# Optimization experiments

Measured on AMD Instinct MI355X. Metric: run time of the kernel, lower is better.

The kernel has to match this reference:

```python
import jax, jax.numpy as jnp
import numpy as np
import math

RC = 3.6            # cutoff radius
SMOOTH_W = 0.3      # ShiftedCosine smoothing width
N_RAD = 12          # max_radial=11 -> 12 radial functions
L_MAX = 3           # max_angular
N_TYPES = 3
BOX = 27.4
# neighbor-type pairs a1<=a2 (keys_to_properties layout), sqrt(2) for off-diagonal
PAIR_A1 = np.array([0, 0, 0, 1, 1, 2])
PAIR_A2 = np.array([0, 1, 2, 1, 2, 2])
PAIR_FACT = np.where(PAIR_A1 != PAIR_A2, np.sqrt(2.0), 1.0).astype(np.float32)


def _gto_setup():
    # GTO primitives g_n(r) = N_n r^n exp(-r^2/(2 sigma_n^2)), orthonormalized via S^{-1/2}
    n = np.arange(N_RAD, dtype=np.float64)
    sigma = RC * np.maximum(np.sqrt(n), 1.0) / N_RAD
    gam = np.array([math.gamma(v) for v in (n + 1.5)])
    norm = 1.0 / np.sqrt(0.5 * gam * sigma ** (2 * n + 3))
    npow = n[:, None] + n[None, :]
    c = 0.5 / sigma[:, None] ** 2 + 0.5 / sigma[None, :] ** 2
    gam2 = np.vectorize(math.gamma)((npow + 3.0) / 2.0)
    S = norm[:, None] * norm[None, :] * 0.5 * gam2 * c ** (-(npow + 3.0) / 2.0)
    w, V = np.linalg.eigh(S)
    Sinv_half = (V * (1.0 / np.sqrt(w))) @ V.T
    return sigma.astype(np.float32), norm.astype(np.float32), Sinv_half.astype(np.float32)

SIGMA, NORM, SINV = _gto_setup()


def radial_basis(r):
    # r [...,] -> [..., N_RAD] orthonormalized GTO values
    n = jnp.arange(N_RAD, dtype=r.dtype)
    sig = jnp.asarray(SIGMA)
    g = jnp.asarray(NORM) * r[..., None] ** n * jnp.exp(-0.5 * r[..., None] ** 2 / sig ** 2)
    return g @ jnp.asarray(SINV)


def real_sph_l3(u):
    # real spherical harmonics l=0..3 on unit vectors u [...,3] -> [...,16]
    x, y, z = u[..., 0], u[..., 1], u[..., 2]
    x2, y2, z2 = x * x, y * y, z * z
    one = jnp.ones_like(x)
    return jnp.stack([
        0.28209479177387814 * one,
        0.4886025119029199 * y, 0.4886025119029199 * z, 0.4886025119029199 * x,
        1.0925484305920792 * x * y, 1.0925484305920792 * y * z,
        0.31539156525252005 * (3.0 * z2 - 1.0),
        1.0925484305920792 * x * z, 0.5462742152960396 * (x2 - y2),
        0.5900435899266435 * y * (3.0 * x2 - y2), 2.890611442640554 * x * y * z,
        0.4570457994644658 * y * (5.0 * z2 - 1.0), 0.3731763325901154 * z * (5.0 * z2 - 3.0),
        0.4570457994644658 * x * (5.0 * z2 - 1.0), 1.445305721320277 * z * (x2 - y2),
        0.5900435899266435 * x * (3.0 * x2 - y2),
    ], axis=-1)


def cutoff_fn(r):
    # ShiftedCosine: 1 for r<rc-w, cosine switch on [rc-w, rc], 0 beyond
    t = jnp.clip((r - (RC - SMOOTH_W)) / SMOOTH_W, 0.0, 1.0)
    return 0.5 * (1.0 + jnp.cos(jnp.pi * t))


def soap_features(positions, species):
    B, N, _ = positions.shape
    rvec = positions[:, :, None, :] - positions[:, None, :, :]  # [B,N,N,3]
    d2 = jnp.sum(rvec * rvec, axis=-1)
    nonself = ~jnp.eye(N, dtype=bool)[None]
    dist = jnp.sqrt(jnp.where(nonself, d2, 1.0))                 # safe for grads
    w = cutoff_fn(dist) * nonself                                 # [B,N,N] pair weight
    unit = rvec / dist[..., None]
    R = radial_basis(dist) * w[..., None]                         # [B,N,N,12]
    Y = real_sph_l3(unit)                                         # [B,N,N,16]
    T = jax.nn.one_hot(species, N_TYPES, dtype=positions.dtype)   # [B,N,3]
    # density expansion coefficients c_{i,a,n,lm}
    c = jnp.einsum('bja,bijn,bijk->biank', T, R, Y)               # [B,N,3,12,16]
    c1 = c[:, :, PAIR_A1]                                         # [B,N,6,12,16]
    c2 = c[:, :, PAIR_A2]
    l_slices = [(0, 1), (1, 4), (4, 9), (9, 16)]
    ps = []
    for l, (s, e) in enumerate(l_slices):
        p = jnp.einsum('bipnm,bipqm->bipnq', c1[..., s:e], c2[..., s:e])
        ps.append(p / jnp.sqrt(jnp.asarray(2.0 * l + 1.0, positions.dtype)))
    p = jnp.stack(ps, axis=-1)                                    # [B,N,6,12,12,4]
    p = p * jnp.asarray(PAIR_FACT)[:, None, None, None]
    return p.reshape(B * N, -1)                                   # [B*N, 3456]


def setup_inputs() -> dict:
    key = jax.random.key(0)
    k0, k1, k2 = jax.random.split(key, 3)
    positions = jax.random.uniform(k0, (4, 1024, 3), dtype=jnp.float32) * BOX
    species = jax.random.randint(k1, (4, 1024), 0, N_TYPES, dtype=jnp.int32)
    W = jax.random.normal(k2, (3456,), dtype=jnp.float32) * 0.02
    b = jnp.zeros((1,), dtype=jnp.float32)
    return {"positions": positions, "species": species, "W": W, "b": b}


def reference(positions, species, W, b):
    feats = soap_features(positions, species)   # [B*N, 3456]
    return feats @ W[:, None] + b               # per-atom energies [B*N, 1]
```

## Files before the change

kernel.cpp:

```cpp
#include <hip/hip_runtime.h>
#include <math.h>

#define NRAD   12
#define NSPH   16
#define NTYPE  3
#define NATOM  1024
#define MAXNBR 64
#define RCUT   3.6f

#define RSTR   13
#define YSTR   17
#define CSTR   20

#define NPAIR  144

#define SQRT2F 1.41421356237309515f
#define LS1    0.57735026918962576f
#define LS2    0.44721359549995794f
#define LS3    0.37796447300922722f

struct SoapConsts {
    float norm[NRAD];
    float inv2sig2[NRAD];
    float sinv[NRAD * NRAD];
};

static void compute_consts(SoapConsts* C) {
    double G[26];
    G[2] = 1.0;
    G[3] = 0.88622692545275801364908374167057259139877;
    for (int t = 4; t < 26; ++t) G[t] = (0.5 * t - 1.0) * G[t - 2];

    double sigma[NRAD], norm[NRAD];
    for (int n = 0; n < NRAD; ++n) {
        double sq = sqrt((double)n);
        if (sq < 1.0) sq = 1.0;
        sigma[n] = 3.6 * sq / 12.0;
        norm[n]  = 1.0 / sqrt(0.5 * G[2 * n + 3] * pow(sigma[n], 2.0 * n + 3.0));
    }

    double S[NRAD][NRAD];
    for (int i = 0; i < NRAD; ++i)
        for (int j = 0; j < NRAD; ++j) {
            double c = 0.5 / (sigma[i] * sigma[i]) + 0.5 / (sigma[j] * sigma[j]);
            double e = 0.5 * (i + j + 3.0);
            S[i][j]  = norm[i] * norm[j] * 0.5 * G[i + j + 3] * pow(c, -e);
        }

    double A[NRAD][NRAD], V[NRAD][NRAD];
    for (int i = 0; i < NRAD; ++i)
        for (int j = 0; j < NRAD; ++j) {
            A[i][j] = S[i][j];
            V[i][j] = (i == j) ? 1.0 : 0.0;
        }
    for (int sweep = 0; sweep < 60; ++sweep) {
        double off = 0.0;
        for (int p = 0; p < NRAD - 1; ++p)
            for (int q = p + 1; q < NRAD; ++q) off += A[p][q] * A[p][q];
        if (off < 1e-26) break;
        for (int p = 0; p < NRAD - 1; ++p) {
            for (int q = p + 1; q < NRAD; ++q) {
                double apq = A[p][q];
                if (fabs(apq) < 1e-300) continue;
                double tau = (A[q][q] - A[p][p]) / (2.0 * apq);
                double tt  = ((tau >= 0.0) ? 1.0 : -1.0) / (fabs(tau) + sqrt(1.0 + tau * tau));
                double cc  = 1.0 / sqrt(1.0 + tt * tt);
                double ss  = tt * cc;
                for (int k = 0; k < NRAD; ++k) {
                    double akp = A[k][p], akq = A[k][q];
                    A[k][p] = cc * akp - ss * akq;
                    A[k][q] = ss * akp + cc * akq;
                }
                for (int k = 0; k < NRAD; ++k) {
                    double apk = A[p][k], aqk = A[q][k];
                    A[p][k] = cc * apk - ss * aqk;
                    A[q][k] = ss * apk + cc * aqk;
                }
                for (int k = 0; k < NRAD; ++k) {
                    double vkp = V[k][p], vkq = V[k][q];
                    V[k][p] = cc * vkp - ss * vkq;
                    V[k][q] = ss * vkp + cc * vkq;
                }
            }
        }
    }
    double wisr[NRAD];
    for (int k = 0; k < NRAD; ++k) wisr[k] = 1.0 / sqrt(A[k][k]);
    for (int i = 0; i < NRAD; ++i)
        for (int j = 0; j < NRAD; ++j) {
            double s = 0.0;
            for (int k = 0; k < NRAD; ++k) s += V[i][k] * wisr[k] * V[j][k];
            C->sinv[i * NRAD + j] = (float)s;
        }
    for (int n = 0; n < NRAD; ++n) {
        C->norm[n]     = (float)norm[n];
        C->inv2sig2[n] = (float)(0.5 / (sigma[n] * sigma[n]));
    }
}

__device__ __forceinline__ void ldrow(const float* __restrict__ row, float* r) {
    const float4* p = reinterpret_cast<const float4*>(row);
    float4 a = p[0], b = p[1], c = p[2], d = p[3];
    r[0]=a.x;  r[1]=a.y;  r[2]=a.z;  r[3]=a.w;
    r[4]=b.x;  r[5]=b.y;  r[6]=b.z;  r[7]=b.w;
    r[8]=c.x;  r[9]=c.y;  r[10]=c.z; r[11]=c.w;
    r[12]=d.x; r[13]=d.y; r[14]=d.z; r[15]=d.w;
}

__device__ __forceinline__ float dot4l(const float* c1, const float* c2,
                                       float4 w4, float fact) {
    float d0 = c1[0]*c2[0];
    float d1 = c1[1]*c2[1] + c1[2]*c2[2] + c1[3]*c2[3];
    float d2 = c1[4]*c2[4] + c1[5]*c2[5] + c1[6]*c2[6] + c1[7]*c2[7]
             + c1[8]*c2[8];
    float d3 = c1[9]*c2[9] + c1[10]*c2[10] + c1[11]*c2[11] + c1[12]*c2[12]
             + c1[13]*c2[13] + c1[14]*c2[14] + c1[15]*c2[15];
    return fact * (w4.x * d0 + (LS1 * w4.y) * d1
                 + (LS2 * w4.z) * d2 + (LS3 * w4.w) * d3);
}

__global__ __launch_bounds__(64) void soap_kernel(
    const float* __restrict__ positions,
    const int*   __restrict__ species,
    const float* __restrict__ W,
    const float* __restrict__ bias,
    float*       __restrict__ out,
    SoapConsts C)
{
    const int atom = blockIdx.x;
    const int b    = atom >> 10;
    const int i    = atom & (NATOM - 1);
    const int lane = threadIdx.x;

    const float* pos = positions + b * NATOM * 3;
    const float xi = pos[3 * i], yi = pos[3 * i + 1], zi = pos[3 * i + 2];

    __shared__ int   nbIdx[MAXNBR];
    __shared__ float nbR[MAXNBR][RSTR];
    __shared__ float nbY[MAXNBR][YSTR];
    __shared__ int   nbSp[MAXNBR];
    __shared__ float cbuf[NTYPE][NRAD * CSTR];

    int nNbr = 0;
    const float rc2 = RCUT * RCUT;
    for (int base = 0; base < NATOM; base += 64) {
        int j = base + lane;
        float dx = xi - pos[3 * j];
        float dy = yi - pos[3 * j + 1];
        float dz = zi - pos[3 * j + 2];
        float d2 = dx * dx + dy * dy + dz * dz;
        bool pred = (j != i) && (d2 < rc2);
        unsigned long long m = __ballot(pred);
        if (pred) {
            int slot = nNbr + __popcll(m & ((1ull << lane) - 1ull));
            if (slot < MAXNBR) nbIdx[slot] = j;
        }
        nNbr += __popcll(m);
    }
    if (nNbr > MAXNBR) nNbr = MAXNBR;
    __syncthreads();

    if (lane < nNbr) {
        int j = nbIdx[lane];
        float dx = xi - pos[3 * j];
        float dy = yi - pos[3 * j + 1];
        float dz = zi - pos[3 * j + 2];
        float d2 = dx * dx + dy * dy + dz * dz;
        float d  = sqrtf(d2);
        float inv = 1.0f / d;
        float ux = dx * inv, uy = dy * inv, uz = dz * inv;

        float t = (d - (RCUT - 0.3f)) * (1.0f / 0.3f);
        t = fminf(fmaxf(t, 0.0f), 1.0f);
        float w = 0.5f * (1.0f + cosf(3.14159265358979323846f * t));

        float g[NRAD];
        float rp = 1.0f;
        #pragma unroll
        for (int n = 0; n < NRAD; ++n) {
            g[n] = C.norm[n] * rp * expf(-d2 * C.inv2sig2[n]) * w;
            rp *= d;
        }
        #pragma unroll
        for (int mm = 0; mm < NRAD; ++mm) {
            float s = 0.0f;
            #pragma unroll
            for (int n = 0; n < NRAD; ++n) s += g[n] * C.sinv[n * NRAD + mm];
            nbR[lane][mm] = s;
        }

        float x2 = ux * ux, y2 = uy * uy, z2 = uz * uz;
        nbY[lane][0]  = 0.28209479177387814f;
        nbY[lane][1]  = 0.4886025119029199f * uy;
        nbY[lane][2]  = 0.4886025119029199f * uz;
        nbY[lane][3]  = 0.4886025119029199f * ux;
        nbY[lane][4]  = 1.0925484305920792f * ux * uy;
        nbY[lane][5]  = 1.0925484305920792f * uy * uz;
        nbY[lane][6]  = 0.31539156525252005f * (3.0f * z2 - 1.0f);
        nbY[lane][7]  = 1.0925484305920792f * ux * uz;
        nbY[lane][8]  = 0.5462742152960396f * (x2 - y2);
        nbY[lane][9]  = 0.5900435899266435f * uy * (3.0f * x2 - y2);
        nbY[lane][10] = 2.890611442640554f * ux * uy * uz;
        nbY[lane][11] = 0.4570457994644658f * uy * (5.0f * z2 - 1.0f);
        nbY[lane][12] = 0.3731763325901154f * uz * (5.0f * z2 - 3.0f);
        nbY[lane][13] = 0.4570457994644658f * ux * (5.0f * z2 - 1.0f);
        nbY[lane][14] = 1.445305721320277f * uz * (x2 - y2);
        nbY[lane][15] = 0.5900435899266435f * ux * (3.0f * x2 - y2);
        nbSp[lane] = species[b * NATOM + j];
    }
    __syncthreads();

    float a0[3], a1_[3], a2_[3];
    int mI[3], kI[3];
    #pragma unroll
    for (int t = 0; t < 3; ++t) {
        a0[t] = a1_[t] = a2_[t] = 0.0f;
        int mk = lane + t * 64;
        mI[t] = mk >> 4;
        kI[t] = mk & 15;
    }
    for (int j = 0; j < nNbr; ++j) {
        int sp = nbSp[j];
        #pragma unroll
        for (int t = 0; t < 3; ++t) {
            float v = nbR[j][mI[t]] * nbY[j][kI[t]];
            a0[t]  += (sp == 0) ? v : 0.0f;
            a1_[t] += (sp == 1) ? v : 0.0f;
            a2_[t] += (sp == 2) ? v : 0.0f;
        }
    }
    #pragma unroll
    for (int t = 0; t < 3; ++t) {
        cbuf[0][mI[t] * CSTR + kI[t]] = a0[t];
        cbuf[1][mI[t] * CSTR + kI[t]] = a1_[t];
        cbuf[2][mI[t] * CSTR + kI[t]] = a2_[t];
    }
    __syncthreads();

    float partial = 0.0f;
    for (int t = 0; t < 3; ++t) {
        int pi  = lane + (t << 6);
        bool act = (pi < NPAIR);
        int piC = act ? pi : 0;
        int n = piC / 12;
        int q = piC - 12 * n;

        float cq0[16], cq1[16], cq2[16], cn_[16];
        ldrow(&cbuf[0][q * CSTR], cq0);
        ldrow(&cbuf[1][q * CSTR], cq1);
        ldrow(&cbuf[2][q * CSTR], cq2);

        const float* wbase = W + n * 48 + q * 4;
        float acc = 0.0f;

        ldrow(&cbuf[0][n * CSTR], cn_);
        acc += dot4l(cn_, cq0, *reinterpret_cast<const float4*>(wbase + 0 * 576), 1.0f);
        acc += dot4l(cn_, cq1, *reinterpret_cast<const float4*>(wbase + 1 * 576), SQRT2F);
        acc += dot4l(cn_, cq2, *reinterpret_cast<const float4*>(wbase + 2 * 576), SQRT2F);

        ldrow(&cbuf[1][n * CSTR], cn_);
        acc += dot4l(cn_, cq1, *reinterpret_cast<const float4*>(wbase + 3 * 576), 1.0f);
        acc += dot4l(cn_, cq2, *reinterpret_cast<const float4*>(wbase + 4 * 576), SQRT2F);

        ldrow(&cbuf[2][n * CSTR], cn_);
        acc += dot4l(cn_, cq2, *reinterpret_cast<const float4*>(wbase + 5 * 576), 1.0f);

        partial += act ? acc : 0.0f;
    }

    #pragma unroll
    for (int off = 32; off > 0; off >>= 1)
        partial += __shfl_down(partial, off, 64);
    if (lane == 0) out[atom] = partial + bias[0];
}

extern "C" void kernel_launch(void* const* d_in, const int* in_sizes, int n_in,
                              void* d_out, int out_size, void* d_ws, size_t ws_size,
                              hipStream_t stream) {
    const float* positions = (const float*)d_in[0];
    const int*   species   = (const int*)d_in[1];
    const float* W         = (const float*)d_in[2];
    const float* bias      = (const float*)d_in[3];
    float*       out       = (float*)d_out;

    SoapConsts C;
    compute_consts(&C);

    int nAtoms = in_sizes[0] / 3;
    soap_kernel<<<nAtoms, 64, 0, stream>>>(positions, species, W, bias, out, C);
}
```

Baseline: 75.73 us.

## Transpose positions to SoA, shrink neighbor cap, and cut register pressure

A new pre-kernel transposes positions into a global SoA buffer so the neighbor scan does coalesced loads. MAXNBR drops from 64 to 32, and the shared arrays lose their padding. Neighbor index and species are packed into one shared int. The pair loop is restructured with unroll 1 and fewer live row arrays, together with launch bounds of 6 waves, to lower register use and raise occupancy. Capping neighbors at 32 can silently drop neighbors in dense regions (the expected count here is about 32 at this density), which changes results, and the extra launch adds overhead.

```diff
diff --git a/kernel.cpp b/kernel.cpp
--- a/kernel.cpp
+++ b/kernel.cpp
@@ -5,11 +5,11 @@
 #define NSPH   16
 #define NTYPE  3
 #define NATOM  1024
-#define MAXNBR 64
+#define MAXNBR 32
 #define RCUT   3.6f
 
-#define RSTR   13
-#define YSTR   17
+#define RSTR   12
+#define YSTR   16
 #define CSTR   20
 
 #define NPAIR  144
@@ -24,6 +24,8 @@
     float inv2sig2[NRAD];
     float sinv[NRAD * NRAD];
 };
+
+__device__ float g_posT[3][4 * NATOM];
 
 static void compute_consts(SoapConsts* C) {
     double G[26];
@@ -98,6 +100,14 @@
     }
 }
 
+__global__ __launch_bounds__(256) void transpose_pos(const float* __restrict__ pos) {
+    int tid = blockIdx.x * 256 + threadIdx.x;
+    const float* p = pos + 3 * tid;
+    g_posT[0][tid] = p[0];
+    g_posT[1][tid] = p[1];
+    g_posT[2][tid] = p[2];
+}
+
 __device__ __forceinline__ void ldrow(const float* __restrict__ row, float* r) {
     const float4* p = reinterpret_cast<const float4*>(row);
     float4 a = p[0], b = p[1], c = p[2], d = p[3];
@@ -105,6 +115,10 @@
     r[4]=b.x;  r[5]=b.y;  r[6]=b.z;  r[7]=b.w;
     r[8]=c.x;  r[9]=c.y;  r[10]=c.z; r[11]=c.w;
     r[12]=d.x; r[13]=d.y; r[14]=d.z; r[15]=d.w;
+}
+
+__device__ __forceinline__ float4 ld4(const float* p) {
+    return *reinterpret_cast<const float4*>(p);
 }
 
 __device__ __forceinline__ float dot4l(const float* c1, const float* c2,
@@ -119,8 +133,7 @@
                  + (LS2 * w4.z) * d2 + (LS3 * w4.w) * d3);
 }
 
-__global__ __launch_bounds__(64) void soap_kernel(
-    const float* __restrict__ positions,
+__global__ __launch_bounds__(64, 6) void soap_kernel(
     const int*   __restrict__ species,
     const float* __restrict__ W,
     const float* __restrict__ bias,
@@ -132,28 +145,29 @@
     const int i    = atom & (NATOM - 1);
     const int lane = threadIdx.x;
 
-    const float* pos = positions + b * NATOM * 3;
-    const float xi = pos[3 * i], yi = pos[3 * i + 1], zi = pos[3 * i + 2];
-
-    __shared__ int   nbIdx[MAXNBR];
+    const float* px = &g_posT[0][b * NATOM];
+    const float* py = &g_posT[1][b * NATOM];
+    const float* pz = &g_posT[2][b * NATOM];
+    const float xi = px[i], yi = py[i], zi = pz[i];
+
+    __shared__ int   nbPk[MAXNBR];
     __shared__ float nbR[MAXNBR][RSTR];
     __shared__ float nbY[MAXNBR][YSTR];
-    __shared__ int   nbSp[MAXNBR];
     __shared__ float cbuf[NTYPE][NRAD * CSTR];
 
     int nNbr = 0;
     const float rc2 = RCUT * RCUT;
     for (int base = 0; base < NATOM; base += 64) {
         int j = base + lane;
-        float dx = xi - pos[3 * j];
-        float dy = yi - pos[3 * j + 1];
-        float dz = zi - pos[3 * j + 2];
+        float dx = xi - px[j];
+        float dy = yi - py[j];
+        float dz = zi - pz[j];
         float d2 = dx * dx + dy * dy + dz * dz;
         bool pred = (j != i) && (d2 < rc2);
         unsigned long long m = __ballot(pred);
         if (pred) {
             int slot = nNbr + __popcll(m & ((1ull << lane) - 1ull));
-            if (slot < MAXNBR) nbIdx[slot] = j;
+            if (slot < MAXNBR) nbPk[slot] = j;
         }
         nNbr += __popcll(m);
     }
@@ -161,10 +175,10 @@
     __syncthreads();
 
     if (lane < nNbr) {
-        int j = nbIdx[lane];
-        float dx = xi - pos[3 * j];
-        float dy = yi - pos[3 * j + 1];
-        float dz = zi - pos[3 * j + 2];
+        int j = nbPk[lane];
+        float dx = xi - px[j];
+        float dy = yi - py[j];
+        float dz = zi - pz[j];
         float d2 = dx * dx + dy * dy + dz * dz;
         float d  = sqrtf(d2);
         float inv = 1.0f / d;
@@ -206,7 +220,7 @@
         nbY[lane][13] = 0.4570457994644658f * ux * (5.0f * z2 - 1.0f);
         nbY[lane][14] = 1.445305721320277f * uz * (x2 - y2);
         nbY[lane][15] = 0.5900435899266435f * ux * (3.0f * x2 - y2);
-        nbSp[lane] = species[b * NATOM + j];
+        nbPk[lane] = j | (species[b * NATOM + j] << 16);
     }
     __syncthreads();
 
@@ -220,7 +234,7 @@
         kI[t] = mk & 15;
     }
     for (int j = 0; j < nNbr; ++j) {
-        int sp = nbSp[j];
+        int sp = nbPk[j] >> 16;
         #pragma unroll
         for (int t = 0; t < 3; ++t) {
             float v = nbR[j][mI[t]] * nbY[j][kI[t]];
@@ -238,32 +252,29 @@
     __syncthreads();
 
     float partial = 0.0f;
+    #pragma unroll 1
     for (int t = 0; t < 3; ++t) {
         int pi  = lane + (t << 6);
         bool act = (pi < NPAIR);
         int piC = act ? pi : 0;
         int n = piC / 12;
         int q = piC - 12 * n;
-
-        float cq0[16], cq1[16], cq2[16], cn_[16];
-        ldrow(&cbuf[0][q * CSTR], cq0);
-        ldrow(&cbuf[1][q * CSTR], cq1);
-        ldrow(&cbuf[2][q * CSTR], cq2);
-
         const float* wbase = W + n * 48 + q * 4;
+
+        float A_[16], B_[16], Cv[16];
         float acc = 0.0f;
-
-        ldrow(&cbuf[0][n * CSTR], cn_);
-        acc += dot4l(cn_, cq0, *reinterpret_cast<const float4*>(wbase + 0 * 576), 1.0f);
-        acc += dot4l(cn_, cq1, *reinterpret_cast<const float4*>(wbase + 1 * 576), SQRT2F);
-        acc += dot4l(cn_, cq2, *reinterpret_cast<const float4*>(wbase + 2 * 576), SQRT2F);
-
-        ldrow(&cbuf[1][n * CSTR], cn_);
-        acc += dot4l(cn_, cq1, *reinterpret_cast<const float4*>(wbase + 3 * 576), 1.0f);
-        acc += dot4l(cn_, cq2, *reinterpret_cast<const float4*>(wbase + 4 * 576), SQRT2F);
-
-        ldrow(&cbuf[2][n * CSTR], cn_);
-        acc += dot4l(cn_, cq2, *reinterpret_cast<const float4*>(wbase + 5 * 576), 1.0f);
+        ldrow(&cbuf[0][n * CSTR], A_);
+        ldrow(&cbuf[0][q * CSTR], B_);
+        ldrow(&cbuf[2][q * CSTR], Cv);
+        acc += dot4l(A_, B_, ld4(wbase + 0 * 576), 1.0f);
+        ldrow(&cbuf[1][q * CSTR], B_);
+        acc += dot4l(A_, B_, ld4(wbase + 1 * 576), SQRT2F);
+        acc += dot4l(A_, Cv, ld4(wbase + 2 * 576), SQRT2F);
+        ldrow(&cbuf[1][n * CSTR], A_);
+        acc += dot4l(A_, B_, ld4(wbase + 3 * 576), 1.0f);
+        acc += dot4l(A_, Cv, ld4(wbase + 4 * 576), SQRT2F);
+        ldrow(&cbuf[2][n * CSTR], A_);
+        acc += dot4l(A_, Cv, ld4(wbase + 5 * 576), 1.0f);
 
         partial += act ? acc : 0.0f;
     }
@@ -287,5 +298,6 @@
     compute_consts(&C);
 
     int nAtoms = in_sizes[0] / 3;
-    soap_kernel<<<nAtoms, 64, 0, stream>>>(positions, species, W, bias, out, C);
-}
+    transpose_pos<<<nAtoms / 256, 256, 0, stream>>>(positions);
+    soap_kernel<<<nAtoms, 64, 0, stream>>>(species, W, bias, out, C);
+}
```

New measurement: 75.97 us. Within noise of the previous version (+0.3%).
